# Optimization experiments

Measured on AMD Instinct MI355X. Metric: run time of the kernel, lower is better.

## Reference

```python
import jax, jax.numpy as jnp
import numpy as np

N = 50000          # padded nodes
E_CFG = 800000     # padded cfg edges
E_GKT = 800000     # padded gkt edges
FN = 128           # node feature dim
FE = 128           # gkt edge feature dim
OUT = 128          # out_size (== hidden dim, required by shared Linears)
HEADS = 8
HEAD = OUT // HEADS
DIN = FN + OUT     # input dim to shared Linears


def _seg_softmax(logits, seg_ids, num_segments):
    mx = jax.ops.segment_max(logits, seg_ids, num_segments=num_segments)
    e = jnp.exp(logits - mx[seg_ids])
    s = jax.ops.segment_sum(e, seg_ids, num_segments=num_segments)
    return e / s[seg_ids]


def setup_inputs() -> dict:
    key = jax.random.key(0)
    ks = jax.random.split(key, 16)
    d = {
        'node_fts': jax.random.normal(ks[0], (N, FN), jnp.float32),
        'gkt_edge_fts': jax.random.normal(ks[1], (E_GKT, FE), jnp.float32),
        'hidden': jax.random.normal(ks[2], (N, OUT), jnp.float32),
        'cfg_indices_padded': jax.random.randint(ks[3], (E_CFG, 2), 0, N, jnp.int32),
        'gkt_indices_padded': jax.random.randint(ks[4], (E_GKT, 2), 0, N, jnp.int32),
    }
    sc = 1.0 / np.sqrt(DIN)
    d['W_m'] = jax.random.normal(ks[5], (DIN, OUT), jnp.float32) * sc
    d['b_m'] = jnp.zeros((OUT,), jnp.float32)
    d['W_skip'] = jax.random.normal(ks[6], (DIN, OUT), jnp.float32) * sc
    d['b_skip'] = jnp.zeros((OUT,), jnp.float32)
    d['W_a1'] = jax.random.normal(ks[7], (DIN, HEADS), jnp.float32) * sc
    d['b_a1'] = jnp.zeros((HEADS,), jnp.float32)
    d['W_a2'] = jax.random.normal(ks[8], (DIN, HEADS), jnp.float32) * sc
    d['b_a2'] = jnp.zeros((HEADS,), jnp.float32)
    d['W_ae'] = jax.random.normal(ks[9], (FE, HEADS), jnp.float32) * (1.0 / np.sqrt(FE))
    d['b_ae'] = jnp.zeros((HEADS,), jnp.float32)
    return d


def reference(node_fts, gkt_edge_fts, hidden, cfg_indices_padded, gkt_indices_padded,
              W_m, b_m, W_skip, b_skip, W_a1, b_a1, W_a2, b_a2, W_ae, b_ae):
    nb_nodes = node_fts.shape[0]
    nb_cfg = cfg_indices_padded.shape[0]
    nb_gkt = gkt_indices_padded.shape[0]
    cfg_row, cfg_col = cfg_indices_padded[:, 0], cfg_indices_padded[:, 1]
    gkt_row, gkt_col = gkt_indices_padded[:, 0], gkt_indices_padded[:, 1]

    # ---- cfg pass ----
    cfg_z = jnp.concatenate([node_fts, hidden], axis=-1)           # [N, DIN]
    cfg_att1 = cfg_z @ W_a1 + b_a1                                 # [N, H]
    cfg_att2 = cfg_z @ W_a2 + b_a2
    cfg_logits = cfg_att1[cfg_row] + cfg_att2[cfg_col]             # [E, H]
    cfg_coefs = _seg_softmax(jax.nn.leaky_relu(cfg_logits), cfg_row, nb_cfg)
    cfg_vals = (cfg_z @ W_m + b_m).reshape(nb_nodes, HEADS, HEAD)  # [N, H, hd]
    cfg_msg = cfg_coefs[:, :, None] * cfg_vals[cfg_col]            # [E, H, hd]
    cfg_hidden = jax.ops.segment_sum(cfg_msg, cfg_row, num_segments=nb_nodes)
    cfg_hidden = cfg_hidden.reshape(nb_nodes, OUT)
    cfg_hidden = cfg_hidden + (cfg_z @ W_skip + b_skip)            # residual
    cfg_hidden = jax.nn.relu(cfg_hidden)

    # ---- gkt pass ----
    gkt_z = jnp.concatenate([node_fts, cfg_hidden], axis=-1)       # [N, DIN]
    gkt_att1 = gkt_z @ W_a1 + b_a1
    gkt_att2 = gkt_z @ W_a2 + b_a2
    gkt_att_e = gkt_edge_fts @ W_ae + b_ae                         # [E, H]
    gkt_logits = gkt_att1[gkt_row] + gkt_att2[gkt_col] + gkt_att_e
    gkt_coefs = _seg_softmax(jax.nn.leaky_relu(gkt_logits), gkt_row, nb_gkt)
    gkt_vals = (gkt_z @ W_m + b_m).reshape(nb_nodes, HEADS, HEAD)
    msg = gkt_coefs[:, :, None] * gkt_vals[gkt_col]
    ret = jax.ops.segment_sum(msg, gkt_row, num_segments=nb_nodes)
    ret = ret.reshape(nb_nodes, OUT)
    ret = ret + (gkt_z @ W_skip + b_skip)
    ret = jax.nn.relu(ret)
    return ret
```

## Files before the change

### kernel.cpp

```cpp
#include <hip/hip_runtime.h>

using short8  = __attribute__((ext_vector_type(8))) short;
using floatx4 = __attribute__((ext_vector_type(4))) float;

#define CAP 64

__device__ __forceinline__ unsigned short f2bf(float f) {
    unsigned int u = __float_as_uint(f);
    u += 0x7fffu + ((u >> 16) & 1u);
    return (unsigned short)(u >> 16);
}
__device__ __forceinline__ float bf2f(unsigned short s) {
    return __uint_as_float(((unsigned int)s) << 16);
}

__global__ void k_pack_w(const float* __restrict__ Wm, const float* __restrict__ Wsk,
                         const float* __restrict__ Wa1, const float* __restrict__ Wa2,
                         unsigned short* __restrict__ Wpack, float* __restrict__ Wa) {
    int id = blockIdx.x * 256 + threadIdx.x;
    int col = id >> 8;
    int k = id & 255;
    float v = (col < 128) ? Wm[k * 128 + col] : Wsk[k * 128 + (col - 128)];
    Wpack[col * 256 + k] = f2bf(v);
    if (id < 256 * 16) {
        int kk = id >> 4, j = id & 15;
        Wa[kk * 16 + j] = (j < 8) ? Wa1[kk * 8 + j] : Wa2[kk * 8 + (j - 8)];
    }
}

__global__ void k_zcvt(const float* __restrict__ nf, const float* __restrict__ hid,
                       unsigned short* __restrict__ zbf,
                       int* __restrict__ cur0, int* __restrict__ cur1, int N) {
    int id = blockIdx.x * 256 + threadIdx.x;
    if (id < N) { cur0[id] = id * CAP; cur1[id] = id * CAP; }
    if (id >= N * 32) return;
    int row = id >> 5;
    int c4 = (id & 31) * 4;
    float4 av = *(const float4*)&nf[row * 128 + c4];
    float4 bv = *(const float4*)&hid[row * 128 + c4];
    ushort4 pa; pa.x = f2bf(av.x); pa.y = f2bf(av.y); pa.z = f2bf(av.z); pa.w = f2bf(av.w);
    ushort4 pb; pb.x = f2bf(bv.x); pb.y = f2bf(bv.y); pb.z = f2bf(bv.z); pb.w = f2bf(bv.w);
    *(ushort4*)&zbf[row * 256 + c4] = pa;
    *(ushort4*)&zbf[row * 256 + 128 + c4] = pb;
}

template <int PHASE>
__global__ void k_fill(const int* __restrict__ idx, int* __restrict__ cursor,
                       int* __restrict__ ccol, int2* __restrict__ ce, int E) {
    int e = blockIdx.x * 256 + threadIdx.x;
    if (e >= E) return;
    int r = idx[2 * e], c = idx[2 * e + 1];
    int p = atomicAdd(&cursor[r], 1);
    if (p < r * CAP + CAP) {
        if (PHASE == 0) ccol[p] = c;
        else            { int2 v; v.x = c; v.y = e; ce[p] = v; }
    }
}

__launch_bounds__(256)
__global__ void k_gemm(const unsigned short* __restrict__ zbf,
                       const unsigned short* __restrict__ Wpack,
                       const float* __restrict__ bm, const float* __restrict__ bsk,
                       unsigned short* __restrict__ vals, float* __restrict__ skip, int M) {
    const int colblk = blockIdx.x;
    const int rowBase = blockIdx.y * 128;
    __shared__ short As[128 * 40];
    __shared__ short Bs[128 * 40];
    const int t = threadIdx.x;
    const int wid = t >> 6, lane = t & 63;
    const int wm = wid >> 1, wn = wid & 1;

    floatx4 acc[4][4];
#pragma unroll
    for (int i = 0; i < 4; i++)
#pragma unroll
        for (int j = 0; j < 4; j++) acc[i][j] = (floatx4){0.f, 0.f, 0.f, 0.f};

    const unsigned short* Bbase = Wpack + colblk * 128 * 256;
    const int kq = (lane >> 4) * 8;
    const int rr = lane & 15;

    for (int kt = 0; kt < 256; kt += 32) {
#pragma unroll
        for (int s = 0; s < 2; s++) {
            int ch = t + s * 256;
            int r = ch >> 2, c = ch & 3;
            int gr = rowBase + r; if (gr >= M) gr = M - 1;
            *(int4*)&As[r * 40 + c * 8] = *(const int4*)&zbf[gr * 256 + kt + c * 8];
            *(int4*)&Bs[r * 40 + c * 8] = *(const int4*)&Bbase[r * 256 + kt + c * 8];
        }
        __syncthreads();
        short8 af[4], bfm[4];
#pragma unroll
        for (int i = 0; i < 4; i++) af[i] = *(short8*)&As[(wm * 64 + i * 16 + rr) * 40 + kq];
#pragma unroll
        for (int j = 0; j < 4; j++) bfm[j] = *(short8*)&Bs[(wn * 64 + j * 16 + rr) * 40 + kq];
#pragma unroll
        for (int i = 0; i < 4; i++)
#pragma unroll
            for (int j = 0; j < 4; j++)
                acc[i][j] = __builtin_amdgcn_mfma_f32_16x16x32_bf16(af[i], bfm[j], acc[i][j], 0, 0, 0);
        __syncthreads();
    }

    const int rquad = lane >> 4, cidx = lane & 15;
#pragma unroll
    for (int i = 0; i < 4; i++) {
#pragma unroll
        for (int j = 0; j < 4; j++) {
            int gc = wn * 64 + j * 16 + cidx;
#pragma unroll
            for (int r = 0; r < 4; r++) {
                int gr = rowBase + wm * 64 + i * 16 + rquad * 4 + r;
                if (gr < M) {
                    float v = acc[i][j][r];
                    if (colblk == 0) vals[gr * 128 + gc] = f2bf(v + bm[gc]);
                    else             skip[gr * 128 + gc] = v + bsk[gc];
                }
            }
        }
    }
}

__launch_bounds__(256)
__global__ void k_att(const float* __restrict__ zA, const float* __restrict__ zB,
                      const float* __restrict__ Wa, const float* __restrict__ ba1,
                      const float* __restrict__ ba2, float* __restrict__ att, int N) {
    __shared__ float Ws[4096];
    int t = threadIdx.x;
#pragma unroll
    for (int s = 0; s < 16; s++) Ws[s * 256 + t] = Wa[s * 256 + t];
    __syncthreads();
    int node = blockIdx.x * 256 + t;
    if (node >= N) return;
    float acc[16];
#pragma unroll
    for (int j = 0; j < 16; j++) acc[j] = (j < 8) ? ba1[j] : ba2[j - 8];
    const float* a = &zA[node * 128];
    const float* b = &zB[node * 128];
    for (int k0 = 0; k0 < 128; k0 += 4) {
        float4 v = *(const float4*)&a[k0];
        float vv[4] = {v.x, v.y, v.z, v.w};
#pragma unroll
        for (int r = 0; r < 4; r++) {
            const float* w = &Ws[(k0 + r) * 16];
#pragma unroll
            for (int j = 0; j < 16; j++) acc[j] += vv[r] * w[j];
        }
    }
    for (int k0 = 0; k0 < 128; k0 += 4) {
        float4 v = *(const float4*)&b[k0];
        float vv[4] = {v.x, v.y, v.z, v.w};
#pragma unroll
        for (int r = 0; r < 4; r++) {
            const float* w = &Ws[(128 + k0 + r) * 16];
#pragma unroll
            for (int j = 0; j < 16; j++) acc[j] += vv[r] * w[j];
        }
    }
#pragma unroll
    for (int j = 0; j < 16; j++) att[node * 16 + j] = acc[j];
}

__launch_bounds__(256)
__global__ void k_atte(const float* __restrict__ ef, const float* __restrict__ Wae,
                       const float* __restrict__ bae, float* __restrict__ atte, int E) {
    __shared__ float Ws[1024];
    int t = threadIdx.x;
    for (int s = t; s < 1024; s += 256) Ws[s] = Wae[s];
    __syncthreads();
    int e = blockIdx.x * 256 + t;
    if (e >= E) return;
    float acc[8];
#pragma unroll
    for (int h = 0; h < 8; h++) acc[h] = bae[h];
    const float* row = &ef[e * 128];
    for (int k0 = 0; k0 < 128; k0 += 4) {
        float4 v = *(const float4*)&row[k0];
        float vv[4] = {v.x, v.y, v.z, v.w};
#pragma unroll
        for (int r = 0; r < 4; r++) {
            const float* w = &Ws[(k0 + r) * 8];
#pragma unroll
            for (int h = 0; h < 8; h++) acc[h] += vv[r] * w[h];
        }
    }
    float4 o0 = {acc[0], acc[1], acc[2], acc[3]};
    float4 o1 = {acc[4], acc[5], acc[6], acc[7]};
    *(float4*)&atte[e * 8] = o0;
    *(float4*)&atte[e * 8 + 4] = o1;
}

template <int PHASE>
__launch_bounds__(256)
__global__ void k_agg(const int* __restrict__ cursor,
                      const int* __restrict__ ccol, const int2* __restrict__ ce,
                      const float* __restrict__ att, const unsigned short* __restrict__ vals,
                      const float* __restrict__ skip, const float* __restrict__ atte,
                      unsigned short* __restrict__ zbf, float* __restrict__ cfgh,
                      float* __restrict__ out, int N) {
    int node = (blockIdx.x * 256 + threadIdx.x) >> 6;
    int lane = threadIdx.x & 63;
    if (node >= N) return;
    int h = lane >> 3;
    int f0 = lane * 2;
    float a1 = att[node * 16 + h];
    int base = node * CAP;
    int cnt = cursor[node] - base;
    if (cnt > CAP) cnt = CAP;
    float acc0 = 0.f, acc1 = 0.f, dsum = 0.f;
    for (int s = 0; s < cnt; s++) {
        int col, eid = 0;
        if (PHASE == 0) col = ccol[base + s];
        else { int2 v = ce[base + s]; col = v.x; eid = v.y; }
        float logit = a1 + att[col * 16 + 8 + h];
        if (PHASE == 1) logit += atte[eid * 8 + h];
        float l = (logit >= 0.f) ? logit : 0.01f * logit;
        float w = __expf(l);
        dsum += w;
        unsigned int pv = *(const unsigned int*)&vals[col * 128 + f0];
        acc0 += w * bf2f((unsigned short)(pv & 0xffffu));
        acc1 += w * bf2f((unsigned short)(pv >> 16));
    }
    if (cnt > 0) {
        float inv = 1.f / dsum;
        acc0 *= inv; acc1 *= inv;
    }
    float r0 = acc0 + skip[node * 128 + f0];
    float r1 = acc1 + skip[node * 128 + f0 + 1];
    r0 = r0 > 0.f ? r0 : 0.f;
    r1 = r1 > 0.f ? r1 : 0.f;
    if (PHASE == 0) {
        unsigned int packed = ((unsigned int)f2bf(r1) << 16) | (unsigned int)f2bf(r0);
        *(unsigned int*)&zbf[node * 256 + 128 + f0] = packed;
        float2 fo = {r0, r1};
        *(float2*)&cfgh[node * 128 + f0] = fo;
    } else {
        float2 fo = {r0, r1};
        *(float2*)&out[node * 128 + f0] = fo;
    }
}

extern "C" void kernel_launch(void* const* d_in, const int* in_sizes, int n_in,
                              void* d_out, int out_size, void* d_ws, size_t ws_size,
                              hipStream_t stream) {
    const float* node_fts = (const float*)d_in[0];
    const float* gkt_ef   = (const float*)d_in[1];
    const float* hidden   = (const float*)d_in[2];
    const int*   cfg_idx  = (const int*)d_in[3];
    const int*   gkt_idx  = (const int*)d_in[4];
    const float* W_m  = (const float*)d_in[5];
    const float* b_m  = (const float*)d_in[6];
    const float* W_sk = (const float*)d_in[7];
    const float* b_sk = (const float*)d_in[8];
    const float* W_a1 = (const float*)d_in[9];
    const float* b_a1 = (const float*)d_in[10];
    const float* W_a2 = (const float*)d_in[11];
    const float* b_a2 = (const float*)d_in[12];
    const float* W_ae = (const float*)d_in[13];
    const float* b_ae = (const float*)d_in[14];

    const int N  = in_sizes[0] / 128;
    const int Ec = in_sizes[3] / 2;
    const int Eg = in_sizes[4] / 2;

    char* ws = (char*)d_ws;
    size_t off = 0;
    auto alloc = [&](size_t bytes) -> void* {
        off = (off + 255) & ~(size_t)255;
        void* p = ws + off;
        off += bytes;
        return p;
    };
    unsigned short* zbf   = (unsigned short*)alloc((size_t)N * 256 * 2);
    unsigned short* vals  = (unsigned short*)alloc((size_t)N * 128 * 2);
    float* skip   = (float*)alloc((size_t)N * 128 * 4);
    float* cfgh   = (float*)alloc((size_t)N * 128 * 4);
    float* att    = (float*)alloc((size_t)N * 16 * 4);
    float* atte   = (float*)alloc((size_t)Eg * 8 * 4);
    unsigned short* Wpack = (unsigned short*)alloc(256 * 256 * 2);
    float* Wa     = (float*)alloc(256 * 16 * 4);
    int* cur0     = (int*)alloc((size_t)N * 4);
    int* cur1     = (int*)alloc((size_t)N * 4);
    int* ccol     = (int*)alloc((size_t)N * CAP * 4);
    int2* ce      = (int2*)alloc((size_t)N * CAP * 8);

    dim3 ggrid(2, (N + 127) / 128);

    k_pack_w<<<256, 256, 0, stream>>>(W_m, W_sk, W_a1, W_a2, Wpack, Wa);
    k_zcvt<<<(N * 32 + 255) / 256, 256, 0, stream>>>(node_fts, hidden, zbf, cur0, cur1, N);
    k_atte<<<(Eg + 255) / 256, 256, 0, stream>>>(gkt_ef, W_ae, b_ae, atte, Eg);
    k_fill<1><<<(Eg + 255) / 256, 256, 0, stream>>>(gkt_idx, cur1, nullptr, ce, Eg);

    k_fill<0><<<(Ec + 255) / 256, 256, 0, stream>>>(cfg_idx, cur0, ccol, nullptr, Ec);
    k_gemm<<<ggrid, 256, 0, stream>>>(zbf, Wpack, b_m, b_sk, vals, skip, N);
    k_att<<<(N + 255) / 256, 256, 0, stream>>>(node_fts, hidden, Wa, b_a1, b_a2, att, N);
    k_agg<0><<<(N * 64 + 255) / 256, 256, 0, stream>>>(cur0, ccol, nullptr, att, vals,
                                                       skip, nullptr, zbf, cfgh, nullptr, N);

    k_gemm<<<ggrid, 256, 0, stream>>>(zbf, Wpack, b_m, b_sk, vals, skip, N);
    k_att<<<(N + 255) / 256, 256, 0, stream>>>(node_fts, cfgh, Wa, b_a1, b_a2, att, N);
    k_agg<1><<<(N * 64 + 255) / 256, 256, 0, stream>>>(cur1, nullptr, ce, att, vals,
                                                       skip, atte, nullptr, nullptr,
                                                       (float*)d_out, N);
}
```

Baseline: 1.048 ms.

## Fuse prep and fill kernels; broadcast neighbor indices via wave shuffles in aggregation

Merges weight packing with feature conversion and the two CSR fill kernels into single launches, cutting launch overhead. In the aggregation kernel each lane preloads one neighbor index (and edge id) up front, and the loop fetches them with __shfl instead of a dependent global load per iteration. This shortens the serial memory chain in the gather loop. It relies on CAP equalling the 64-lane wavefront.

```diff
diff --git a/kernel.cpp b/kernel.cpp
--- a/kernel.cpp
+++ b/kernel.cpp
@@ -14,24 +14,23 @@
     return __uint_as_float(((unsigned int)s) << 16);
 }
 
-__global__ void k_pack_w(const float* __restrict__ Wm, const float* __restrict__ Wsk,
-                         const float* __restrict__ Wa1, const float* __restrict__ Wa2,
-                         unsigned short* __restrict__ Wpack, float* __restrict__ Wa) {
-    int id = blockIdx.x * 256 + threadIdx.x;
-    int col = id >> 8;
-    int k = id & 255;
-    float v = (col < 128) ? Wm[k * 128 + col] : Wsk[k * 128 + (col - 128)];
-    Wpack[col * 256 + k] = f2bf(v);
-    if (id < 256 * 16) {
-        int kk = id >> 4, j = id & 15;
-        Wa[kk * 16 + j] = (j < 8) ? Wa1[kk * 8 + j] : Wa2[kk * 8 + (j - 8)];
-    }
-}
-
-__global__ void k_zcvt(const float* __restrict__ nf, const float* __restrict__ hid,
+__global__ void k_prep(const float* __restrict__ Wm, const float* __restrict__ Wsk,
+                       const float* __restrict__ Wa1, const float* __restrict__ Wa2,
+                       unsigned short* __restrict__ Wpack, float* __restrict__ Wa,
+                       const float* __restrict__ nf, const float* __restrict__ hid,
                        unsigned short* __restrict__ zbf,
                        int* __restrict__ cur0, int* __restrict__ cur1, int N) {
     int id = blockIdx.x * 256 + threadIdx.x;
+    if (id < 65536) {
+        int col = id >> 8;
+        int k = id & 255;
+        float v = (col < 128) ? Wm[k * 128 + col] : Wsk[k * 128 + (col - 128)];
+        Wpack[col * 256 + k] = f2bf(v);
+        if (id < 256 * 16) {
+            int kk = id >> 4, j = id & 15;
+            Wa[kk * 16 + j] = (j < 8) ? Wa1[kk * 8 + j] : Wa2[kk * 8 + (j - 8)];
+        }
+    }
     if (id < N) { cur0[id] = id * CAP; cur1[id] = id * CAP; }
     if (id >= N * 32) return;
     int row = id >> 5;
@@ -44,16 +43,19 @@
     *(ushort4*)&zbf[row * 256 + 128 + c4] = pb;
 }
 
-template <int PHASE>
-__global__ void k_fill(const int* __restrict__ idx, int* __restrict__ cursor,
-                       int* __restrict__ ccol, int2* __restrict__ ce, int E) {
+__global__ void k_fill_both(const int* __restrict__ cfg_idx, const int* __restrict__ gkt_idx,
+                            int* __restrict__ cur0, int* __restrict__ cur1,
+                            int* __restrict__ ccol, int2* __restrict__ ce, int Ec, int Eg) {
     int e = blockIdx.x * 256 + threadIdx.x;
-    if (e >= E) return;
-    int r = idx[2 * e], c = idx[2 * e + 1];
-    int p = atomicAdd(&cursor[r], 1);
-    if (p < r * CAP + CAP) {
-        if (PHASE == 0) ccol[p] = c;
-        else            { int2 v; v.x = c; v.y = e; ce[p] = v; }
+    if (e < Ec) {
+        int r = cfg_idx[2 * e], c = cfg_idx[2 * e + 1];
+        int p = atomicAdd(&cur0[r], 1);
+        if (p < r * CAP + CAP) ccol[p] = c;
+    }
+    if (e < Eg) {
+        int r = gkt_idx[2 * e], c = gkt_idx[2 * e + 1];
+        int p = atomicAdd(&cur1[r], 1);
+        if (p < r * CAP + CAP) { int2 v; v.x = c; v.y = e; ce[p] = v; }
     }
 }
 
@@ -204,17 +206,26 @@
     if (node >= N) return;
     int h = lane >> 3;
     int f0 = lane * 2;
-    float a1 = att[node * 16 + h];
     int base = node * CAP;
     int cnt = cursor[node] - base;
     if (cnt > CAP) cnt = CAP;
+    if (cnt < 0) cnt = 0;
+
+    int mycol = 0, myeid = 0;
+    if (lane < cnt) {
+        if (PHASE == 0) mycol = ccol[base + lane];
+        else { int2 v = ce[base + lane]; mycol = v.x; myeid = v.y; }
+    }
+    float a1 = att[node * 16 + h];
     float acc0 = 0.f, acc1 = 0.f, dsum = 0.f;
+#pragma unroll 4
     for (int s = 0; s < cnt; s++) {
-        int col, eid = 0;
-        if (PHASE == 0) col = ccol[base + s];
-        else { int2 v = ce[base + s]; col = v.x; eid = v.y; }
+        int col = __shfl(mycol, s);
         float logit = a1 + att[col * 16 + 8 + h];
-        if (PHASE == 1) logit += atte[eid * 8 + h];
+        if (PHASE == 1) {
+            int eid = __shfl(myeid, s);
+            logit += atte[eid * 8 + h];
+        }
         float l = (logit >= 0.f) ? logit : 0.01f * logit;
         float w = __expf(l);
         dsum += w;
@@ -263,6 +274,7 @@
     const int N  = in_sizes[0] / 128;
     const int Ec = in_sizes[3] / 2;
     const int Eg = in_sizes[4] / 2;
+    const int Emax = (Ec > Eg) ? Ec : Eg;
 
     char* ws = (char*)d_ws;
     size_t off = 0;
@@ -287,12 +299,12 @@
 
     dim3 ggrid(2, (N + 127) / 128);
 
-    k_pack_w<<<256, 256, 0, stream>>>(W_m, W_sk, W_a1, W_a2, Wpack, Wa);
-    k_zcvt<<<(N * 32 + 255) / 256, 256, 0, stream>>>(node_fts, hidden, zbf, cur0, cur1, N);
+    k_prep<<<(N * 32 + 255) / 256, 256, 0, stream>>>(W_m, W_sk, W_a1, W_a2, Wpack, Wa,
+                                                     node_fts, hidden, zbf, cur0, cur1, N);
+    k_fill_both<<<(Emax + 255) / 256, 256, 0, stream>>>(cfg_idx, gkt_idx, cur0, cur1,
+                                                        ccol, ce, Ec, Eg);
     k_atte<<<(Eg + 255) / 256, 256, 0, stream>>>(gkt_ef, W_ae, b_ae, atte, Eg);
-    k_fill<1><<<(Eg + 255) / 256, 256, 0, stream>>>(gkt_idx, cur1, nullptr, ce, Eg);
-
-    k_fill<0><<<(Ec + 255) / 256, 256, 0, stream>>>(cfg_idx, cur0, ccol, nullptr, Ec);
+
     k_gemm<<<ggrid, 256, 0, stream>>>(zbf, Wpack, b_m, b_sk, vals, skip, N);
     k_att<<<(N + 255) / 256, 256, 0, stream>>>(node_fts, hidden, Wa, b_a1, b_a2, att, N);
     k_agg<0><<<(N * 64 + 255) / 256, 256, 0, stream>>>(cur0, ccol, nullptr, att, vals,
```

New measurement: 1.010 ms. 3.6% less time.
